# Kernel optimization log

Hardware: AMD Instinct MI355X
Metric: run time of the kernel (lower is better)

The kernel has to match this reference:

```python
import jax, jax.numpy as jnp
import numpy as np

DIM = 128
NUM_HEADS = 4
WIN = 16  # effective window: window_size(8) * sqrt(dim_t=4)
N = WIN * WIN
B_ = 512
NW = 64


def _relative_position_index(wh, ww):
    coords = np.stack(np.meshgrid(np.arange(wh), np.arange(ww), indexing='ij'))  # (2,wh,ww)
    cf = coords.reshape(2, -1)
    rel = cf[:, :, None] - cf[:, None, :]  # (2,N,N)
    rel = rel.transpose(1, 2, 0).copy()
    rel[:, :, 0] += wh - 1
    rel[:, :, 1] += ww - 1
    rel[:, :, 0] *= 2 * ww - 1
    return rel.sum(-1).astype(np.int32)  # (N,N)


def setup_inputs() -> dict:
    key = jax.random.key(0)
    ks = jax.random.split(key, 7)
    inputs = jax.random.normal(ks[0], (B_, N, DIM), dtype=jnp.float32)
    mask = jax.random.normal(ks[1], (NW, N, N), dtype=jnp.float32)
    qkv_w = jax.random.normal(ks[2], (3 * DIM, DIM), dtype=jnp.float32) * 0.02
    qkv_b = jnp.zeros((3 * DIM,), dtype=jnp.float32)
    proj_w = jax.random.normal(ks[3], (DIM, DIM), dtype=jnp.float32) * 0.02
    proj_b = jnp.zeros((DIM,), dtype=jnp.float32)
    table_sz = (2 * WIN - 1) * (2 * WIN - 1)  # 961
    bias_table = jax.random.normal(ks[4], (table_sz, NUM_HEADS), dtype=jnp.float32) * 0.02
    rel_idx = jnp.asarray(_relative_position_index(WIN, WIN))  # (N,N) int32
    return {"inputs": inputs, "mask": mask, "qkv_w": qkv_w, "qkv_b": qkv_b,
            "proj_w": proj_w, "proj_b": proj_b, "bias_table": bias_table,
            "rel_idx": rel_idx}


def reference(inputs, mask, qkv_w, qkv_b, proj_w, proj_b, bias_table, rel_idx):
    B, Nn, C = inputs.shape
    H = bias_table.shape[1]
    Dh = C // H
    scale = Dh ** -0.5
    qkv = (inputs @ qkv_w.T + qkv_b).reshape(B, Nn, 3, H, Dh)
    qkv = jnp.transpose(qkv, (2, 0, 3, 1, 4))  # (3,B,H,N,Dh)
    q, k, v = qkv[0] * scale, qkv[1], qkv[2]
    attn = jnp.einsum('bhnd,bhmd->bhnm', q, k)  # (B,H,N,N)
    rpb = jnp.transpose(bias_table[rel_idx], (2, 0, 1))  # (H,N,N)
    attn = attn + rpb[None]
    nW = mask.shape[0]
    attn = attn.reshape(B // nW, nW, H, Nn, Nn) + mask[None, :, None]
    attn = jax.nn.softmax(attn.reshape(B, H, Nn, Nn), axis=-1)
    out = jnp.einsum('bhnm,bhmd->bhnd', attn, v)
    out = jnp.transpose(out, (0, 2, 1, 3)).reshape(B, Nn, C)
    return out @ proj_w.T + proj_b
```

## Files before the change

### kernel.cpp

```cpp
#include <hip/hip_runtime.h>

typedef __bf16 bf16;
typedef __bf16 bf16x8 __attribute__((ext_vector_type(8)));
typedef __bf16 bf16x4 __attribute__((ext_vector_type(4)));
typedef float f32x4 __attribute__((ext_vector_type(4)));

static __device__ __forceinline__ f32x4 mfma16(bf16x8 a, bf16x8 b, f32x4 c) {
  return __builtin_amdgcn_mfma_f32_16x16x32_bf16(a, b, c, 0, 0, 0);
}

static __device__ __forceinline__ bf16x8 ld_bf8(const float* __restrict__ p) {
  f32x4 a = *(const f32x4*)p;
  f32x4 b = *(const f32x4*)(p + 4);
  bf16x8 r;
  r[0] = (bf16)a[0]; r[1] = (bf16)a[1]; r[2] = (bf16)a[2]; r[3] = (bf16)a[3];
  r[4] = (bf16)b[0]; r[5] = (bf16)b[1]; r[6] = (bf16)b[2]; r[7] = (bf16)b[3];
  return r;
}

__global__ void k0_rpb(const float* __restrict__ bt, const int* __restrict__ ri,
                       float* __restrict__ rpb) {
  int t = blockIdx.x * 256 + threadIdx.x;
  int idx = ri[t];
  f32x4 v = *(const f32x4*)(bt + idx * 4);
#pragma unroll
  for (int h = 0; h < 4; ++h) rpb[h * 65536 + t] = v[h];
}

__global__ void __launch_bounds__(256, 2)
k1_qkv(const float* __restrict__ x, const float* __restrict__ qw,
       const float* __restrict__ qb, bf16* __restrict__ q_s,
       bf16* __restrict__ k_s, bf16* __restrict__ vt) {
  const int tid = threadIdx.x;
  const int wv = tid >> 6, ln = tid & 15, qd = (tid >> 4) & 3;
  const int b = blockIdx.x >> 1;
  const int row0 = (blockIdx.x & 1) * 128 + (wv >> 1) * 64;
  const int cg = wv & 1;

  bf16x8 xf[4][4];
#pragma unroll
  for (int nt = 0; nt < 4; ++nt)
#pragma unroll
    for (int ks = 0; ks < 4; ++ks)
      xf[nt][ks] = ld_bf8(x + (size_t)(b * 256 + row0 + nt * 16 + ln) * 128 +
                          ks * 32 + qd * 8);

#pragma unroll
  for (int ch = 0; ch < 2; ++ch) {
    f32x4 acc[4][4];
#pragma unroll
    for (int mt = 0; mt < 4; ++mt)
#pragma unroll
      for (int nt = 0; nt < 4; ++nt) acc[mt][nt] = (f32x4){0.f, 0.f, 0.f, 0.f};
#pragma unroll
    for (int mt = 0; mt < 4; ++mt)
#pragma unroll
      for (int ks = 0; ks < 4; ++ks) {
        bf16x8 wf = ld_bf8(qw + (size_t)(ch * 128 + cg * 64 + mt * 16 + ln) * 128 +
                           ks * 32 + qd * 8);
#pragma unroll
        for (int nt = 0; nt < 4; ++nt) acc[mt][nt] = mfma16(wf, xf[nt][ks], acc[mt][nt]);
      }
    bf16* dst = ch ? k_s : q_s;
    const float scl = ch ? 1.0f : 0.17677669529663689f;
#pragma unroll
    for (int mt = 0; mt < 4; ++mt) {
      const int c0 = cg * 64 + mt * 16 + qd * 4;
      f32x4 b4 = *(const f32x4*)(qb + ch * 128 + c0);
      const int hh = c0 >> 5, d0 = c0 & 31;
#pragma unroll
      for (int nt = 0; nt < 4; ++nt) {
        const int nr = row0 + nt * 16 + ln;
        bf16x4 o;
#pragma unroll
        for (int r = 0; r < 4; ++r) o[r] = (bf16)((acc[mt][nt][r] + b4[r]) * scl);
        *(bf16x4*)(dst + (size_t)((b * 4 + hh) * 256 + nr) * 32 + d0) = o;
      }
    }
  }

  f32x4 av[4][4];
#pragma unroll
  for (int nt = 0; nt < 4; ++nt)
#pragma unroll
    for (int mt = 0; mt < 4; ++mt) av[nt][mt] = (f32x4){0.f, 0.f, 0.f, 0.f};
#pragma unroll
  for (int ks = 0; ks < 4; ++ks)
#pragma unroll
    for (int mt = 0; mt < 4; ++mt) {
      bf16x8 wf = ld_bf8(qw + (size_t)(256 + cg * 64 + mt * 16 + ln) * 128 +
                         ks * 32 + qd * 8);
#pragma unroll
      for (int nt = 0; nt < 4; ++nt) av[nt][mt] = mfma16(xf[nt][ks], wf, av[nt][mt]);
    }
#pragma unroll
  for (int nt = 0; nt < 4; ++nt)
#pragma unroll
    for (int mt = 0; mt < 4; ++mt) {
      const int c = cg * 64 + mt * 16 + ln;
      const float bb = qb[256 + c];
      const int hh = c >> 5, dd = c & 31;
      const int n0 = row0 + nt * 16 + qd * 4;
      bf16x4 o;
#pragma unroll
      for (int r = 0; r < 4; ++r) o[r] = (bf16)(av[nt][mt][r] + bb);
      *(bf16x4*)(vt + (size_t)((b * 4 + hh) * 32 + dd) * 256 + n0) = o;
    }
}

__global__ void __launch_bounds__(256, 2)
k2_attn(const bf16* __restrict__ q_s, const bf16* __restrict__ k_s,
        const bf16* __restrict__ vt, const float* __restrict__ mask,
        const float* __restrict__ rpb, float* __restrict__ ao) {
  __shared__ bf16 ksm[256 * 32];
  __shared__ bf16 vsm[32 * 256];
  __shared__ bf16 psm[4 * 16 * 256];
  const int tid = threadIdx.x, wv = tid >> 6;
  const int ln = tid & 15, qd = (tid >> 4) & 3;
  const int w = blockIdx.x & 63, h = (blockIdx.x >> 6) & 3, rh = blockIdx.x >> 8;

  bf16x4 cmb[2][16];
#pragma unroll
  for (int si = 0; si < 2; ++si) {
    const int n = (rh * 8 + wv * 2 + si) * 16 + ln;
#pragma unroll
    for (int mt = 0; mt < 16; ++mt) {
      f32x4 m4 = *(const f32x4*)(mask + (size_t)(w * 256 + n) * 256 + mt * 16 + qd * 4);
      f32x4 r4 = *(const f32x4*)(rpb + (size_t)h * 65536 + n * 256 + mt * 16 + qd * 4);
      bf16x4 cv;
#pragma unroll
      for (int r = 0; r < 4; ++r) cv[r] = (bf16)(m4[r] + r4[r]);
      cmb[si][mt] = cv;
    }
  }

  for (int ib = 0; ib < 8; ++ib) {
    const int b = w + ib * 64;
    const bf16* kp = k_s + (size_t)(b * 4 + h) * 8192;
    const bf16* vp = vt + (size_t)(b * 4 + h) * 8192;
    __syncthreads();
#pragma unroll
    for (int i = 0; i < 4; ++i) {
      const int ci = i * 256 + tid;
      {
        const int r_ = ci >> 2, cb = ci & 3;
        *(bf16x8*)(ksm + r_ * 32 + ((cb ^ (r_ & 3)) * 8)) =
            *(const bf16x8*)(kp + r_ * 32 + cb * 8);
      }
      {
        const int r_ = ci >> 5, cb = ci & 31;
        *(bf16x8*)(vsm + r_ * 256 + ((cb ^ (r_ & 7)) * 8)) =
            *(const bf16x8*)(vp + r_ * 256 + cb * 8);
      }
    }
    __syncthreads();

#pragma unroll
    for (int si = 0; si < 2; ++si) {
      const int s = rh * 8 + wv * 2 + si;
      bf16x8 qf = *(const bf16x8*)(q_s + (size_t)(b * 4 + h) * 8192 +
                                   (s * 16 + ln) * 32 + qd * 8);
      f32x4 acc[16];
#pragma unroll
      for (int mt = 0; mt < 16; ++mt) acc[mt] = (f32x4){0.f, 0.f, 0.f, 0.f};
#pragma unroll
      for (int mt = 0; mt < 16; ++mt) {
        const int m = mt * 16 + ln;
        bf16x8 af = *(const bf16x8*)(ksm + m * 32 + ((qd ^ (m & 3)) * 8));
        acc[mt] = mfma16(af, qf, acc[mt]);
      }
      float sum = 0.f;
      bf16* pb = psm + wv * 4096 + ln * 256;
#pragma unroll
      for (int mt = 0; mt < 16; ++mt) {
        bf16x4 pv;
#pragma unroll
        for (int r = 0; r < 4; ++r) {
          float p = __expf(acc[mt][r] + (float)cmb[si][mt][r]);
          sum += p;
          pv[r] = (bf16)p;
        }
        *(bf16x4*)(pb + (((mt * 2 + (qd >> 1)) ^ (ln & 7)) * 8) + (qd & 1) * 4) = pv;
      }
      sum += __shfl_xor(sum, 16);
      sum += __shfl_xor(sum, 32);
      const float linv = 1.0f / sum;

      f32x4 accO[2];
      accO[0] = (f32x4){0.f, 0.f, 0.f, 0.f};
      accO[1] = (f32x4){0.f, 0.f, 0.f, 0.f};
#pragma unroll
      for (int kt = 0; kt < 8; ++kt) {
        bf16x8 pf = *(const bf16x8*)(pb + (((kt * 4 + qd) ^ (ln & 7)) * 8));
#pragma unroll
        for (int ct = 0; ct < 2; ++ct) {
          const int d = ct * 16 + ln;
          bf16x8 vf = *(const bf16x8*)(vsm + d * 256 + (((kt * 4 + qd) ^ (d & 7)) * 8));
          accO[ct] = mfma16(pf, vf, accO[ct]);
        }
      }
#pragma unroll
      for (int r = 0; r < 4; ++r) {
        const float lb = __shfl(linv, qd * 4 + r);
        const size_t orow = (size_t)(b * 256 + s * 16 + qd * 4 + r) * 128 + h * 32;
#pragma unroll
        for (int ct = 0; ct < 2; ++ct)
          ao[orow + ct * 16 + ln] = accO[ct][r] * lb;
      }
    }
  }
}

__global__ void __launch_bounds__(256, 2)
k3_proj(const float* __restrict__ xin, const float* __restrict__ pw,
        const float* __restrict__ pbias, float* __restrict__ out) {
  const int tid = threadIdx.x;
  const int wv = tid >> 6, ln = tid & 15, qd = (tid >> 4) & 3;
  const int cg = wv & 1;
  const size_t row0 = (size_t)blockIdx.x * 128 + (wv >> 1) * 64;

  bf16x8 xf[4][4];
#pragma unroll
  for (int nt = 0; nt < 4; ++nt)
#pragma unroll
    for (int ks = 0; ks < 4; ++ks)
      xf[nt][ks] = ld_bf8(xin + (row0 + nt * 16 + ln) * 128 + ks * 32 + qd * 8);
  __syncthreads();

  f32x4 acc[4][4];
#pragma unroll
  for (int mt = 0; mt < 4; ++mt)
#pragma unroll
    for (int nt = 0; nt < 4; ++nt) acc[mt][nt] = (f32x4){0.f, 0.f, 0.f, 0.f};
#pragma unroll
  for (int mt = 0; mt < 4; ++mt)
#pragma unroll
    for (int ks = 0; ks < 4; ++ks) {
      bf16x8 wf = ld_bf8(pw + (size_t)(cg * 64 + mt * 16 + ln) * 128 + ks * 32 + qd * 8);
#pragma unroll
      for (int nt = 0; nt < 4; ++nt) acc[mt][nt] = mfma16(wf, xf[nt][ks], acc[mt][nt]);
    }
#pragma unroll
  for (int mt = 0; mt < 4; ++mt) {
    const int c0 = cg * 64 + mt * 16 + qd * 4;
    f32x4 b4 = *(const f32x4*)(pbias + c0);
#pragma unroll
    for (int nt = 0; nt < 4; ++nt) {
      f32x4 o;
#pragma unroll
      for (int r = 0; r < 4; ++r) o[r] = acc[mt][nt][r] + b4[r];
      *(f32x4*)(out + (row0 + nt * 16 + ln) * 128 + c0) = o;
    }
  }
}

extern "C" void kernel_launch(void* const* d_in, const int* in_sizes, int n_in,
                              void* d_out, int out_size, void* d_ws, size_t ws_size,
                              hipStream_t stream) {
  const float* x = (const float*)d_in[0];
  const float* mask = (const float*)d_in[1];
  const float* qkv_w = (const float*)d_in[2];
  const float* qkv_b = (const float*)d_in[3];
  const float* proj_w = (const float*)d_in[4];
  const float* proj_b = (const float*)d_in[5];
  const float* bias_table = (const float*)d_in[6];
  const int* rel_idx = (const int*)d_in[7];

  char* ws = (char*)d_ws;
  bf16* q_s = (bf16*)ws;
  bf16* k_s = (bf16*)(ws + 33554432);
  bf16* vt = (bf16*)(ws + 2ll * 33554432);
  float* rpb = (float*)(ws + 3ll * 33554432);
  float* ao = (float*)d_out;

  k0_rpb<<<dim3(256), dim3(256), 0, stream>>>(bias_table, rel_idx, rpb);
  k1_qkv<<<dim3(1024), dim3(256), 0, stream>>>(x, qkv_w, qkv_b, q_s, k_s, vt);
  k2_attn<<<dim3(512), dim3(256), 0, stream>>>(q_s, k_s, vt, mask, rpb, ao);
  k3_proj<<<dim3(1024), dim3(256), 0, stream>>>(ao, proj_w, proj_b, (float*)d_out);
}
```

Baseline: 307.6 us.

## Pre-convert weights to bf16, stage inputs in LDS, restructure attention kernel

Adds a kernel that converts the QKV and projection weights to bf16 once, so the GEMM kernels load bf16 weights instead of converting fp32 on every load. The QKV and projection kernels now stage the input tile in swizzled shared memory, read fragments from it per k-step, and raise the occupancy target to three blocks. K and V^T are written pre-swizzled so the attention kernel can copy them linearly into LDS, with the next batch's K/V prefetched into registers. The attention grid doubles to one 16-row strip per wave, with the key loop split into halves to cut register and LDS use. This trades more blocks re-loading mask and bias against better latency hiding and occupancy.

```diff
diff --git a/kernel.cpp b/kernel.cpp
--- a/kernel.cpp
+++ b/kernel.cpp
@@ -9,9 +9,7 @@
   return __builtin_amdgcn_mfma_f32_16x16x32_bf16(a, b, c, 0, 0, 0);
 }
 
-static __device__ __forceinline__ bf16x8 ld_bf8(const float* __restrict__ p) {
-  f32x4 a = *(const f32x4*)p;
-  f32x4 b = *(const f32x4*)(p + 4);
+static __device__ __forceinline__ bf16x8 pk8(f32x4 a, f32x4 b) {
   bf16x8 r;
   r[0] = (bf16)a[0]; r[1] = (bf16)a[1]; r[2] = (bf16)a[2]; r[3] = (bf16)a[3];
   r[4] = (bf16)b[0]; r[5] = (bf16)b[1]; r[6] = (bf16)b[2]; r[7] = (bf16)b[3];
@@ -27,41 +25,57 @@
   for (int h = 0; h < 4; ++h) rpb[h * 65536 + t] = v[h];
 }
 
-__global__ void __launch_bounds__(256, 2)
-k1_qkv(const float* __restrict__ x, const float* __restrict__ qw,
+__global__ void k0_w(const float* __restrict__ qw, const float* __restrict__ pw,
+                     bf16* __restrict__ wqb, bf16* __restrict__ wpb) {
+  int t = blockIdx.x * 256 + threadIdx.x;
+  if (t < 49152) wqb[t] = (bf16)qw[t];
+  else wpb[t - 49152] = (bf16)pw[t - 49152];
+}
+
+__global__ void __launch_bounds__(256, 3)
+k1_qkv(const float* __restrict__ x, const bf16* __restrict__ wqb,
        const float* __restrict__ qb, bf16* __restrict__ q_s,
        bf16* __restrict__ k_s, bf16* __restrict__ vt) {
+  __shared__ bf16 xsm[16384];
   const int tid = threadIdx.x;
   const int wv = tid >> 6, ln = tid & 15, qd = (tid >> 4) & 3;
-  const int b = blockIdx.x >> 1;
-  const int row0 = (blockIdx.x & 1) * 128 + (wv >> 1) * 64;
-  const int cg = wv & 1;
-
-  bf16x8 xf[4][4];
-#pragma unroll
-  for (int nt = 0; nt < 4; ++nt)
-#pragma unroll
-    for (int ks = 0; ks < 4; ++ks)
-      xf[nt][ks] = ld_bf8(x + (size_t)(b * 256 + row0 + nt * 16 + ln) * 128 +
-                          ks * 32 + qd * 8);
+  const int b = blockIdx.x >> 1, half = blockIdx.x & 1;
+  const int rg = wv >> 1, cg = wv & 1;
+
+#pragma unroll
+  for (int j = 0; j < 8; ++j) {
+    const int bidx = j * 256 + tid;
+    const int row = bidx >> 4, c = bidx & 15;
+    const float* g = x + (size_t)(b * 256 + half * 128 + row) * 128 + c * 8;
+    f32x4 a = *(const f32x4*)g, b2 = *(const f32x4*)(g + 4);
+    *(bf16x8*)(xsm + row * 128 + ((c ^ (row & 7)) * 8)) = pk8(a, b2);
+  }
+  __syncthreads();
+
+  f32x4 acc[4][4];
+  bf16x8 xfk[4];
 
 #pragma unroll
   for (int ch = 0; ch < 2; ++ch) {
-    f32x4 acc[4][4];
 #pragma unroll
     for (int mt = 0; mt < 4; ++mt)
 #pragma unroll
       for (int nt = 0; nt < 4; ++nt) acc[mt][nt] = (f32x4){0.f, 0.f, 0.f, 0.f};
 #pragma unroll
-    for (int mt = 0; mt < 4; ++mt)
-#pragma unroll
-      for (int ks = 0; ks < 4; ++ks) {
-        bf16x8 wf = ld_bf8(qw + (size_t)(ch * 128 + cg * 64 + mt * 16 + ln) * 128 +
-                           ks * 32 + qd * 8);
-#pragma unroll
-        for (int nt = 0; nt < 4; ++nt) acc[mt][nt] = mfma16(wf, xf[nt][ks], acc[mt][nt]);
-      }
-    bf16* dst = ch ? k_s : q_s;
+    for (int ks = 0; ks < 4; ++ks) {
+#pragma unroll
+      for (int nt = 0; nt < 4; ++nt) {
+        const int row_l = rg * 64 + nt * 16 + ln;
+        xfk[nt] = *(const bf16x8*)(xsm + row_l * 128 + (((ks * 4 + qd) ^ (ln & 7)) * 8));
+      }
+#pragma unroll
+      for (int mt = 0; mt < 4; ++mt) {
+        bf16x8 wf = *(const bf16x8*)(wqb + (size_t)(ch * 128 + cg * 64 + mt * 16 + ln) * 128 +
+                                     ks * 32 + qd * 8);
+#pragma unroll
+        for (int nt = 0; nt < 4; ++nt) acc[mt][nt] = mfma16(wf, xfk[nt], acc[mt][nt]);
+      }
+    }
     const float scl = ch ? 1.0f : 0.17677669529663689f;
 #pragma unroll
     for (int mt = 0; mt < 4; ++mt) {
@@ -70,29 +84,40 @@
       const int hh = c0 >> 5, d0 = c0 & 31;
 #pragma unroll
       for (int nt = 0; nt < 4; ++nt) {
-        const int nr = row0 + nt * 16 + ln;
+        const int nr = half * 128 + rg * 64 + nt * 16 + ln;
         bf16x4 o;
 #pragma unroll
         for (int r = 0; r < 4; ++r) o[r] = (bf16)((acc[mt][nt][r] + b4[r]) * scl);
-        *(bf16x4*)(dst + (size_t)((b * 4 + hh) * 256 + nr) * 32 + d0) = o;
-      }
-    }
-  }
-
-  f32x4 av[4][4];
+        const size_t base = (size_t)(b * 4 + hh) * 8192;
+        if (ch == 0) {
+          *(bf16x4*)(q_s + base + nr * 32 + d0) = o;
+        } else {
+          const int cb = (d0 >> 3) ^ (nr & 3) ^ ((nr >> 2) & 3);
+          *(bf16x4*)(k_s + base + nr * 32 + cb * 8 + (d0 & 7)) = o;
+        }
+      }
+    }
+  }
+
 #pragma unroll
   for (int nt = 0; nt < 4; ++nt)
 #pragma unroll
-    for (int mt = 0; mt < 4; ++mt) av[nt][mt] = (f32x4){0.f, 0.f, 0.f, 0.f};
-#pragma unroll
-  for (int ks = 0; ks < 4; ++ks)
+    for (int mt = 0; mt < 4; ++mt) acc[nt][mt] = (f32x4){0.f, 0.f, 0.f, 0.f};
+#pragma unroll
+  for (int ks = 0; ks < 4; ++ks) {
+#pragma unroll
+    for (int nt = 0; nt < 4; ++nt) {
+      const int row_l = rg * 64 + nt * 16 + ln;
+      xfk[nt] = *(const bf16x8*)(xsm + row_l * 128 + (((ks * 4 + qd) ^ (ln & 7)) * 8));
+    }
 #pragma unroll
     for (int mt = 0; mt < 4; ++mt) {
-      bf16x8 wf = ld_bf8(qw + (size_t)(256 + cg * 64 + mt * 16 + ln) * 128 +
-                         ks * 32 + qd * 8);
-#pragma unroll
-      for (int nt = 0; nt < 4; ++nt) av[nt][mt] = mfma16(xf[nt][ks], wf, av[nt][mt]);
-    }
+      bf16x8 wf = *(const bf16x8*)(wqb + (size_t)(256 + cg * 64 + mt * 16 + ln) * 128 +
+                                   ks * 32 + qd * 8);
+#pragma unroll
+      for (int nt = 0; nt < 4; ++nt) acc[nt][mt] = mfma16(xfk[nt], wf, acc[nt][mt]);
+    }
+  }
 #pragma unroll
   for (int nt = 0; nt < 4; ++nt)
 #pragma unroll
@@ -100,146 +125,166 @@
       const int c = cg * 64 + mt * 16 + ln;
       const float bb = qb[256 + c];
       const int hh = c >> 5, dd = c & 31;
-      const int n0 = row0 + nt * 16 + qd * 4;
+      const int n0 = half * 128 + rg * 64 + nt * 16 + qd * 4;
       bf16x4 o;
 #pragma unroll
-      for (int r = 0; r < 4; ++r) o[r] = (bf16)(av[nt][mt][r] + bb);
-      *(bf16x4*)(vt + (size_t)((b * 4 + hh) * 32 + dd) * 256 + n0) = o;
-    }
-}
-
-__global__ void __launch_bounds__(256, 2)
+      for (int r = 0; r < 4; ++r) o[r] = (bf16)(acc[nt][mt][r] + bb);
+      const int p = (n0 >> 3) ^ (dd & 7);
+      *(bf16x4*)(vt + (size_t)(b * 4 + hh) * 8192 + dd * 256 + p * 8 + (n0 & 7)) = o;
+    }
+}
+
+__global__ void __launch_bounds__(256, 3)
 k2_attn(const bf16* __restrict__ q_s, const bf16* __restrict__ k_s,
         const bf16* __restrict__ vt, const float* __restrict__ mask,
         const float* __restrict__ rpb, float* __restrict__ ao) {
-  __shared__ bf16 ksm[256 * 32];
-  __shared__ bf16 vsm[32 * 256];
-  __shared__ bf16 psm[4 * 16 * 256];
+  __shared__ bf16 ksm[8192];
+  __shared__ bf16 vsm[8192];
+  __shared__ bf16 psm[8192];
   const int tid = threadIdx.x, wv = tid >> 6;
   const int ln = tid & 15, qd = (tid >> 4) & 3;
   const int w = blockIdx.x & 63, h = (blockIdx.x >> 6) & 3, rh = blockIdx.x >> 8;
-
-  bf16x4 cmb[2][16];
-#pragma unroll
-  for (int si = 0; si < 2; ++si) {
-    const int n = (rh * 8 + wv * 2 + si) * 16 + ln;
+  const int s = rh * 4 + wv;
+  const int swzk = qd ^ (ln & 3) ^ ((ln >> 2) & 3);
+
+  bf16x4 cmb[16];
+  {
+    const int n = s * 16 + ln;
 #pragma unroll
     for (int mt = 0; mt < 16; ++mt) {
-      f32x4 m4 = *(const f32x4*)(mask + (size_t)(w * 256 + n) * 256 + mt * 16 + qd * 4);
+      f32x4 m4 = *(const f32x4*)(mask + ((size_t)w * 256 + n) * 256 + mt * 16 + qd * 4);
       f32x4 r4 = *(const f32x4*)(rpb + (size_t)h * 65536 + n * 256 + mt * 16 + qd * 4);
       bf16x4 cv;
 #pragma unroll
       for (int r = 0; r < 4; ++r) cv[r] = (bf16)(m4[r] + r4[r]);
-      cmb[si][mt] = cv;
+      cmb[mt] = cv;
+    }
+  }
+
+  bf16x8 kr[4], vr[4];
+  {
+    const size_t base = (size_t)(w * 4 + h) * 8192;
+#pragma unroll
+    for (int i = 0; i < 4; ++i) {
+      kr[i] = *(const bf16x8*)(k_s + base + i * 2048 + tid * 8);
+      vr[i] = *(const bf16x8*)(vt + base + i * 2048 + tid * 8);
     }
   }
 
   for (int ib = 0; ib < 8; ++ib) {
     const int b = w + ib * 64;
-    const bf16* kp = k_s + (size_t)(b * 4 + h) * 8192;
-    const bf16* vp = vt + (size_t)(b * 4 + h) * 8192;
     __syncthreads();
 #pragma unroll
     for (int i = 0; i < 4; ++i) {
-      const int ci = i * 256 + tid;
-      {
-        const int r_ = ci >> 2, cb = ci & 3;
-        *(bf16x8*)(ksm + r_ * 32 + ((cb ^ (r_ & 3)) * 8)) =
-            *(const bf16x8*)(kp + r_ * 32 + cb * 8);
-      }
-      {
-        const int r_ = ci >> 5, cb = ci & 31;
-        *(bf16x8*)(vsm + r_ * 256 + ((cb ^ (r_ & 7)) * 8)) =
-            *(const bf16x8*)(vp + r_ * 256 + cb * 8);
-      }
+      *(bf16x8*)(ksm + i * 2048 + tid * 8) = kr[i];
+      *(bf16x8*)(vsm + i * 2048 + tid * 8) = vr[i];
     }
     __syncthreads();
-
-#pragma unroll
-    for (int si = 0; si < 2; ++si) {
-      const int s = rh * 8 + wv * 2 + si;
-      bf16x8 qf = *(const bf16x8*)(q_s + (size_t)(b * 4 + h) * 8192 +
-                                   (s * 16 + ln) * 32 + qd * 8);
-      f32x4 acc[16];
-#pragma unroll
-      for (int mt = 0; mt < 16; ++mt) acc[mt] = (f32x4){0.f, 0.f, 0.f, 0.f};
-#pragma unroll
-      for (int mt = 0; mt < 16; ++mt) {
-        const int m = mt * 16 + ln;
-        bf16x8 af = *(const bf16x8*)(ksm + m * 32 + ((qd ^ (m & 3)) * 8));
-        acc[mt] = mfma16(af, qf, acc[mt]);
-      }
-      float sum = 0.f;
-      bf16* pb = psm + wv * 4096 + ln * 256;
-#pragma unroll
-      for (int mt = 0; mt < 16; ++mt) {
+    if (ib < 7) {
+      const size_t base = (size_t)((w + (ib + 1) * 64) * 4 + h) * 8192;
+#pragma unroll
+      for (int i = 0; i < 4; ++i) {
+        kr[i] = *(const bf16x8*)(k_s + base + i * 2048 + tid * 8);
+        vr[i] = *(const bf16x8*)(vt + base + i * 2048 + tid * 8);
+      }
+    }
+
+    bf16x8 qf = *(const bf16x8*)(q_s + (size_t)(b * 4 + h) * 8192 + (s * 16 + ln) * 32 + qd * 8);
+    float sum = 0.f;
+    f32x4 accO[2];
+    accO[0] = (f32x4){0.f, 0.f, 0.f, 0.f};
+    accO[1] = (f32x4){0.f, 0.f, 0.f, 0.f};
+    bf16* pb = psm + wv * 2048 + ln * 128;
+
+#pragma unroll
+    for (int hk = 0; hk < 2; ++hk) {
+      f32x4 acc[8];
+#pragma unroll
+      for (int i = 0; i < 8; ++i) acc[i] = (f32x4){0.f, 0.f, 0.f, 0.f};
+#pragma unroll
+      for (int i = 0; i < 8; ++i) {
+        const int m = (hk * 8 + i) * 16 + ln;
+        bf16x8 af = *(const bf16x8*)(ksm + m * 32 + swzk * 8);
+        acc[i] = mfma16(af, qf, acc[i]);
+      }
+#pragma unroll
+      for (int i = 0; i < 8; ++i) {
+        const int mt = hk * 8 + i;
         bf16x4 pv;
 #pragma unroll
         for (int r = 0; r < 4; ++r) {
-          float p = __expf(acc[mt][r] + (float)cmb[si][mt][r]);
+          float p = __expf(acc[i][r] + (float)cmb[mt][r]);
           sum += p;
           pv[r] = (bf16)p;
         }
-        *(bf16x4*)(pb + (((mt * 2 + (qd >> 1)) ^ (ln & 7)) * 8) + (qd & 1) * 4) = pv;
-      }
-      sum += __shfl_xor(sum, 16);
-      sum += __shfl_xor(sum, 32);
-      const float linv = 1.0f / sum;
-
-      f32x4 accO[2];
-      accO[0] = (f32x4){0.f, 0.f, 0.f, 0.f};
-      accO[1] = (f32x4){0.f, 0.f, 0.f, 0.f};
-#pragma unroll
-      for (int kt = 0; kt < 8; ++kt) {
+        const int p16 = (i * 2 + (qd >> 1)) ^ (ln & 7);
+        *(bf16x4*)(pb + p16 * 8 + (qd & 1) * 4) = pv;
+      }
+#pragma unroll
+      for (int kt = 0; kt < 4; ++kt) {
         bf16x8 pf = *(const bf16x8*)(pb + (((kt * 4 + qd) ^ (ln & 7)) * 8));
 #pragma unroll
         for (int ct = 0; ct < 2; ++ct) {
           const int d = ct * 16 + ln;
-          bf16x8 vf = *(const bf16x8*)(vsm + d * 256 + (((kt * 4 + qd) ^ (d & 7)) * 8));
+          const int p32 = ((hk * 4 + kt) * 4 + qd) ^ (d & 7);
+          bf16x8 vf = *(const bf16x8*)(vsm + d * 256 + p32 * 8);
           accO[ct] = mfma16(pf, vf, accO[ct]);
         }
       }
-#pragma unroll
-      for (int r = 0; r < 4; ++r) {
-        const float lb = __shfl(linv, qd * 4 + r);
-        const size_t orow = (size_t)(b * 256 + s * 16 + qd * 4 + r) * 128 + h * 32;
-#pragma unroll
-        for (int ct = 0; ct < 2; ++ct)
-          ao[orow + ct * 16 + ln] = accO[ct][r] * lb;
-      }
-    }
-  }
-}
-
-__global__ void __launch_bounds__(256, 2)
-k3_proj(const float* __restrict__ xin, const float* __restrict__ pw,
+    }
+    sum += __shfl_xor(sum, 16);
+    sum += __shfl_xor(sum, 32);
+    const float linv = 1.0f / sum;
+#pragma unroll
+    for (int r = 0; r < 4; ++r) {
+      const float lb = __shfl(linv, qd * 4 + r);
+      const size_t orow = (size_t)(b * 256 + s * 16 + qd * 4 + r) * 128 + h * 32;
+#pragma unroll
+      for (int ct = 0; ct < 2; ++ct) ao[orow + ct * 16 + ln] = accO[ct][r] * lb;
+    }
+  }
+}
+
+__global__ void __launch_bounds__(256, 3)
+k3_proj(const float* __restrict__ xin, const bf16* __restrict__ wpb,
         const float* __restrict__ pbias, float* __restrict__ out) {
+  __shared__ bf16 xsm[16384];
   const int tid = threadIdx.x;
   const int wv = tid >> 6, ln = tid & 15, qd = (tid >> 4) & 3;
-  const int cg = wv & 1;
-  const size_t row0 = (size_t)blockIdx.x * 128 + (wv >> 1) * 64;
-
-  bf16x8 xf[4][4];
-#pragma unroll
-  for (int nt = 0; nt < 4; ++nt)
-#pragma unroll
-    for (int ks = 0; ks < 4; ++ks)
-      xf[nt][ks] = ld_bf8(xin + (row0 + nt * 16 + ln) * 128 + ks * 32 + qd * 8);
+  const int rg = wv >> 1, cg = wv & 1;
+  const size_t row0 = (size_t)blockIdx.x * 128;
+
+#pragma unroll
+  for (int j = 0; j < 8; ++j) {
+    const int bidx = j * 256 + tid;
+    const int row = bidx >> 4, c = bidx & 15;
+    const float* g = xin + (row0 + row) * 128 + c * 8;
+    f32x4 a = *(const f32x4*)g, b2 = *(const f32x4*)(g + 4);
+    *(bf16x8*)(xsm + row * 128 + ((c ^ (row & 7)) * 8)) = pk8(a, b2);
+  }
   __syncthreads();
 
   f32x4 acc[4][4];
+  bf16x8 xfk[4];
 #pragma unroll
   for (int mt = 0; mt < 4; ++mt)
 #pragma unroll
     for (int nt = 0; nt < 4; ++nt) acc[mt][nt] = (f32x4){0.f, 0.f, 0.f, 0.f};
 #pragma unroll
-  for (int mt = 0; mt < 4; ++mt)
-#pragma unroll
-    for (int ks = 0; ks < 4; ++ks) {
-      bf16x8 wf = ld_bf8(pw + (size_t)(cg * 64 + mt * 16 + ln) * 128 + ks * 32 + qd * 8);
-#pragma unroll
-      for (int nt = 0; nt < 4; ++nt) acc[mt][nt] = mfma16(wf, xf[nt][ks], acc[mt][nt]);
-    }
+  for (int ks = 0; ks < 4; ++ks) {
+#pragma unroll
+    for (int nt = 0; nt < 4; ++nt) {
+      const int row_l = rg * 64 + nt * 16 + ln;
+      xfk[nt] = *(const bf16x8*)(xsm + row_l * 128 + (((ks * 4 + qd) ^ (ln & 7)) * 8));
+    }
+#pragma unroll
+    for (int mt = 0; mt < 4; ++mt) {
+      bf16x8 wf = *(const bf16x8*)(wpb + (size_t)(cg * 64 + mt * 16 + ln) * 128 +
+                                   ks * 32 + qd * 8);
+#pragma unroll
+      for (int nt = 0; nt < 4; ++nt) acc[mt][nt] = mfma16(wf, xfk[nt], acc[mt][nt]);
+    }
+  }
 #pragma unroll
   for (int mt = 0; mt < 4; ++mt) {
     const int c0 = cg * 64 + mt * 16 + qd * 4;
@@ -249,7 +294,7 @@
       f32x4 o;
 #pragma unroll
       for (int r = 0; r < 4; ++r) o[r] = acc[mt][nt][r] + b4[r];
-      *(f32x4*)(out + (row0 + nt * 16 + ln) * 128 + c0) = o;
+      *(f32x4*)(out + (row0 + rg * 64 + nt * 16 + ln) * 128 + c0) = o;
     }
   }
 }
@@ -268,13 +313,16 @@
 
   char* ws = (char*)d_ws;
   bf16* q_s = (bf16*)ws;
-  bf16* k_s = (bf16*)(ws + 33554432);
-  bf16* vt = (bf16*)(ws + 2ll * 33554432);
-  float* rpb = (float*)(ws + 3ll * 33554432);
+  bf16* k_s = (bf16*)(ws + 33554432ll);
+  bf16* vt = (bf16*)(ws + 67108864ll);
+  float* rpb = (float*)(ws + 100663296ll);
+  bf16* wqb = (bf16*)(ws + 101711872ll);
+  bf16* wpb = wqb + 49152;
   float* ao = (float*)d_out;
 
   k0_rpb<<<dim3(256), dim3(256), 0, stream>>>(bias_table, rel_idx, rpb);
-  k1_qkv<<<dim3(1024), dim3(256), 0, stream>>>(x, qkv_w, qkv_b, q_s, k_s, vt);
-  k2_attn<<<dim3(512), dim3(256), 0, stream>>>(q_s, k_s, vt, mask, rpb, ao);
-  k3_proj<<<dim3(1024), dim3(256), 0, stream>>>(ao, proj_w, proj_b, (float*)d_out);
-}
+  k0_w<<<dim3(256), dim3(256), 0, stream>>>(qkv_w, proj_w, wqb, wpb);
+  k1_qkv<<<dim3(1024), dim3(256), 0, stream>>>(x, wqb, qkv_b, q_s, k_s, vt);
+  k2_attn<<<dim3(1024), dim3(256), 0, stream>>>(q_s, k_s, vt, mask, rpb, ao);
+  k3_proj<<<dim3(1024), dim3(256), 0, stream>>>(ao, wpb, proj_b, (float*)d_out);
+}
```

New measurement: 311.5 us. About the same (+1.3%).
